# Optimization experiments

Hardware: AMD Instinct MI355X
Metric: run time of the kernel (lower is better)

Reference implementation:

```python
import jax, jax.numpy as jnp
import numpy as np

N, E = 50000, 400000
IN_DIM, TIME_DIM, OUT_DIM, H = 192, 64, 256, 4
D = OUT_DIM // H            # 64 per-head dim
GAT_IN = IN_DIM + TIME_DIM  # 256 == OUT_DIM -> identity residual path


def setup_inputs() -> dict:
    key = jax.random.key(0)
    ks = jax.random.split(key, 9)
    h = jax.random.normal(ks[0], (N, IN_DIM), jnp.float32)
    time_tensor = jax.random.uniform(ks[1], (E,), jnp.float32) * 100.0
    src = jax.random.randint(ks[2], (E,), 0, N, dtype=jnp.int32)
    dst = jax.random.randint(ks[3], (E,), 0, N, dtype=jnp.int32)
    time_w = jax.random.normal(ks[4], (TIME_DIM,), jnp.float32)
    time_b = jax.random.normal(ks[5], (TIME_DIM,), jnp.float32)
    fc_w = jax.random.normal(ks[6], (GAT_IN, H * D), jnp.float32) / np.float32(np.sqrt(GAT_IN))
    attn_l = jax.random.normal(ks[7], (H, D), jnp.float32) * 0.1
    attn_r = jax.random.normal(ks[8], (H, D), jnp.float32) * 0.1
    return {"h": h, "time_tensor": time_tensor, "src": src, "dst": dst,
            "time_w": time_w, "time_b": time_b, "fc_w": fc_w,
            "attn_l": attn_l, "attn_r": attn_r}


def reference(h, time_tensor, src, dst, time_w, time_b, fc_w, attn_l, attn_r):
    # --- temporal encoding per edge: cos(t * w + b) ---
    time_emb = jnp.cos(time_tensor[:, None] * time_w[None, :] + time_b[None, :])  # [E, T]
    # --- mean-aggregate incoming edge time features to nodes (fn.copy_e + fn.mean) ---
    deg = jax.ops.segment_sum(jnp.ones((E,), h.dtype), dst, num_segments=N)       # [N]
    agg_time = jax.ops.segment_sum(time_emb, dst, num_segments=N)
    agg_time = agg_time / jnp.maximum(deg, 1.0)[:, None]                          # [N, T]
    # --- concat node features with aggregated time features ---
    combined = jnp.concatenate([h, agg_time], axis=1)                             # [N, GAT_IN]
    # --- GAT projection and per-node attention logits ---
    feat = (combined @ fc_w).reshape(N, H, D)                                     # [N, H, D]
    el = jnp.einsum('nhd,hd->nh', feat, attn_l)                                   # [N, H]
    er = jnp.einsum('nhd,hd->nh', feat, attn_r)                                   # [N, H]
    # --- edge attention: u_add_v + leaky_relu ---
    e = jax.nn.leaky_relu(el[src] + er[dst], negative_slope=0.01)                 # [E, H]
    # --- edge_softmax over destination segments (numerically stable) ---
    emax = jax.lax.stop_gradient(jax.ops.segment_max(e, dst, num_segments=N))
    emax = jnp.where(jnp.isfinite(emax), emax, 0.0)
    ex = jnp.exp(e - emax[dst])
    denom = jax.ops.segment_sum(ex, dst, num_segments=N)
    a = ex / jnp.maximum(denom[dst], 1e-16)                                       # [E, H]
    # --- u_mul_e + sum aggregation ---
    msg = feat[src] * a[:, :, None]                                               # [E, H, D]
    rst = jax.ops.segment_sum(msg, dst, num_segments=N)                           # [N, H, D]
    # --- identity residual (in_feats == out_feats*num_heads) + elu ---
    rst = rst + combined.reshape(N, H, D)
    rst = jax.nn.elu(rst)
    return rst.reshape(N, OUT_DIM)
```

## Files before the change

kernel.cpp:

```cpp
#include <hip/hip_runtime.h>
#include <hip/hip_bf16.h>
#include <math.h>

#define N_NODES 50000
#define NP      50176
#define N_EDGES 400000
#define IN_DIM  192
#define NB      196

typedef float        f32x4 __attribute__((ext_vector_type(4)));
typedef unsigned int u32x4 __attribute__((ext_vector_type(4)));

__device__ __forceinline__ unsigned short f2bf(float f) {
    union { float f; unsigned int u; } v; v.f = f;
    unsigned int r = (v.u + 0x7FFF + ((v.u >> 16) & 1)) >> 16;
    return (unsigned short)r;
}
__device__ __forceinline__ float bfu_lo(unsigned int u) {
    union { unsigned int u; float f; } v; v.u = u << 16;
    return v.f;
}
__device__ __forceinline__ float bfu_hi(unsigned int u) {
    union { unsigned int u; float f; } v; v.u = u & 0xFFFF0000u;
    return v.f;
}

#define MFMA_BF16(acc, a, b) \
    asm("v_mfma_f32_16x16x32_bf16 %0, %1, %2, %0" : "+v"(acc) : "v"(a), "v"(b))

__global__ void k_hist(const int* __restrict__ dst, int* __restrict__ deg) {
    int e = blockIdx.x * 256 + threadIdx.x;
    if (e >= N_EDGES) return;
    atomicAdd(&deg[dst[e]], 1);
}

__global__ __launch_bounds__(256) void k_scanA(const int* __restrict__ deg,
                                               int* __restrict__ total,
                                               int* __restrict__ start,
                                               int* __restrict__ cursor) {
    __shared__ int part[256];
    __shared__ int base_s;
    int t = threadIdx.x;
    int i = blockIdx.x * 256 + t;
    int v = (i < N_NODES) ? deg[i] : 0;
    part[t] = v;
    __syncthreads();
#pragma unroll
    for (int off = 1; off < 256; off <<= 1) {
        int u = (t >= off) ? part[t - off] : 0;
        __syncthreads();
        part[t] += u;
        __syncthreads();
    }
    if (t == 255) base_s = atomicAdd(total, part[255]);
    __syncthreads();
    if (i < N_NODES) {
        int ex = base_s + part[t] - v;
        start[i] = ex;
        cursor[i] = ex;
    }
}

__global__ void k_bucket(const int* __restrict__ src, const int* __restrict__ dst,
                         const float* __restrict__ time_t, int* __restrict__ cursor,
                         int2* __restrict__ csr2) {
    int e = blockIdx.x * 256 + threadIdx.x;
    if (e >= N_EDGES) return;
    int d = dst[e];
    int idx = atomicAdd(&cursor[d], 1);
    csr2[idx] = make_int2(src[e], __float_as_int(time_t[e]));
}

__global__ void k_prep_w(const float* __restrict__ fw, unsigned short* __restrict__ wF) {
    int tid = blockIdx.x * 256 + threadIdx.x;
    int lane = tid & 63;
    int ks = (tid >> 6) & 7;
    int nt = tid >> 9;
    int c = lane & 15, g = lane >> 4;
    int n = nt * 16 + c;
    int k0 = ks * 32 + g * 8;
    union { unsigned short s[8]; u32x4 v; } u;
#pragma unroll
    for (int j = 0; j < 8; ++j) u.s[j] = f2bf(fw[(size_t)(k0 + j) * 256 + n]);
    *(u32x4*)(wF + (size_t)tid * 8) = u.v;
}

__global__ __launch_bounds__(256) void k_prep_a(const unsigned short* __restrict__ comb,
                                                unsigned short* __restrict__ aF) {
    int tid = blockIdx.x * 256 + threadIdx.x;
    int lane = tid & 63;
    int ks = (tid >> 6) & 7;
    int t = tid >> 9;
    int c = lane & 15, g = lane >> 4;
    u32x4 v = *(const u32x4*)(comb + (size_t)(t * 16 + c) * 256 + ks * 32 + g * 8);
    *(u32x4*)(aF + (size_t)tid * 8) = v;
}

__global__ void k_node_time(const float* __restrict__ h, const int2* __restrict__ csr2,
                            const int* __restrict__ start, const int* __restrict__ deg,
                            const float* __restrict__ tw, const float* __restrict__ tb,
                            unsigned short* __restrict__ comb) {
    int lane = threadIdx.x & 63;
    int wv   = threadIdx.x >> 6;
    int d = blockIdx.x * 4 + wv;
    if (d >= N_NODES) return;
    int k0 = start[d], dg = deg[d];
    float w = tw[lane], b = tb[lane];
    float s = 0.f;
    for (int kc = 0; kc < dg; kc += 64) {
        int cd = min(64, dg - kc);
        float tv = 0.f;
        if (lane < cd) tv = __int_as_float(csr2[k0 + kc + lane].y);
        for (int j = 0; j < cd; ++j) {
            float tj = __shfl(tv, j, 64);
            s += __cosf(tj * w + b);
        }
    }
    float mean = s / fmaxf((float)dg, 1.0f);
    const float* hr = h + (size_t)d * IN_DIM;
    unsigned short* orow = comb + (size_t)d * 256;
    orow[lane]       = f2bf(hr[lane]);
    orow[lane + 64]  = f2bf(hr[lane + 64]);
    orow[lane + 128] = f2bf(hr[lane + 128]);
    orow[lane + 192] = f2bf(mean);
}

__device__ __forceinline__ void gemm_epi(const f32x4 acc[16], int row_lo, int c,
                                         const float* __restrict__ al,
                                         const float* __restrict__ ar,
                                         unsigned short* __restrict__ feat,
                                         float* __restrict__ el,
                                         float* __restrict__ er) {
#pragma unroll
    for (int nt = 0; nt < 16; ++nt) {
#pragma unroll
        for (int reg = 0; reg < 4; ++reg) {
            feat[(size_t)(row_lo + reg) * 256 + nt * 16 + c] = f2bf(acc[nt][reg]);
        }
    }
#pragma unroll
    for (int hh = 0; hh < 4; ++hh) {
        float xl[4] = {0.f, 0.f, 0.f, 0.f};
        float xr[4] = {0.f, 0.f, 0.f, 0.f};
#pragma unroll
        for (int ntl = 0; ntl < 4; ++ntl) {
            int nt = hh * 4 + ntl;
            float av = al[nt * 16 + c];
            float rv = ar[nt * 16 + c];
#pragma unroll
            for (int reg = 0; reg < 4; ++reg) {
                xl[reg] += acc[nt][reg] * av;
                xr[reg] += acc[nt][reg] * rv;
            }
        }
#pragma unroll
        for (int reg = 0; reg < 4; ++reg) {
#pragma unroll
            for (int off = 1; off < 16; off <<= 1) {
                xl[reg] += __shfl_xor(xl[reg], off, 64);
                xr[reg] += __shfl_xor(xr[reg], off, 64);
            }
        }
        if (c == 0) {
#pragma unroll
            for (int reg = 0; reg < 4; ++reg) {
                el[(row_lo + reg) * 4 + hh] = xl[reg];
                er[(row_lo + reg) * 4 + hh] = xr[reg];
            }
        }
    }
}

__global__ __launch_bounds__(512) void k_gemm_mfma(
        const unsigned short* __restrict__ aF,
        const unsigned short* __restrict__ wF,
        const float* __restrict__ al, const float* __restrict__ ar,
        unsigned short* __restrict__ feat,
        float* __restrict__ el, float* __restrict__ er) {
    int lane = threadIdx.x & 63;
    int wave = threadIdx.x >> 6;
    int t0 = blockIdx.x * 16 + wave;
    int c = lane & 15;
    int g = lane >> 4;

    f32x4 acc0[16], acc1[16];
#pragma unroll
    for (int nt = 0; nt < 16; ++nt) {
        acc0[nt] = (f32x4){0.f, 0.f, 0.f, 0.f};
        acc1[nt] = (f32x4){0.f, 0.f, 0.f, 0.f};
    }

    const unsigned short* a0p = aF + ((size_t)(t0 * 8) * 64 + lane) * 8;
    const unsigned short* a1p = aF + ((size_t)((t0 + 8) * 8) * 64 + lane) * 8;
    const unsigned short* bp  = wF + (size_t)lane * 8;

    for (int ks = 0; ks < 8; ++ks) {
        u32x4 a0 = *(const u32x4*)(a0p + ks * 512);
        u32x4 a1 = *(const u32x4*)(a1p + ks * 512);
#pragma unroll
        for (int nt = 0; nt < 16; ++nt) {
            u32x4 b = *(const u32x4*)(bp + (size_t)(nt * 8 + ks) * 512);
            MFMA_BF16(acc0[nt], a0, b);
            MFMA_BF16(acc1[nt], a1, b);
        }
    }

    int row_lo = t0 * 16 + g * 4;
    gemm_epi(acc0, row_lo,       c, al, ar, feat, el, er);
    gemm_epi(acc1, row_lo + 128, c, al, ar, feat, el, er);
}

#define CHUNK 64
__global__ __launch_bounds__(256) void k_node_agg(
        const int2* __restrict__ csr2,
        const int* __restrict__ start, const int* __restrict__ deg,
        const unsigned short* __restrict__ feat, const unsigned short* __restrict__ comb,
        const float* __restrict__ el, const float* __restrict__ er,
        float* __restrict__ out) {
    __shared__ float ex_lds[4][CHUNK * 4];
    __shared__ int   src_lds[4][CHUNK];
    int lane = threadIdx.x & 63;
    int wv   = threadIdx.x >> 6;
    int d = blockIdx.x * 4 + wv;
    int k0 = start[d], k1 = k0 + deg[d];
    int j4 = lane >> 2, h4 = lane & 3;
    int hh = lane >> 4;
    float er_a = er[d * 4 + h4];
    float acc0 = 0.f, acc1 = 0.f, acc2 = 0.f, acc3 = 0.f, den_part = 0.f;

    for (int kc = k0; kc < k1; kc += CHUNK) {
        int cd = min(CHUNK, k1 - kc);
        for (int p = 0; p * 16 < cd; ++p) {
            int j = p * 16 + j4;
            if (j < cd) {
                int s = csr2[kc + j].x;
                if (h4 == 0) src_lds[wv][j] = s;
                float v = el[s * 4 + h4] + er_a;
                v = v > 0.f ? v : 0.01f * v;
                float exv = __expf(v);
                ex_lds[wv][j * 4 + h4] = exv;
                den_part += exv;
            }
        }
#pragma unroll 2
        for (int j = 0; j < cd; ++j) {
            int s = src_lds[wv][j];
            float a = ex_lds[wv][j * 4 + hh];
            const uint2* fp = (const uint2*)(feat + (size_t)s * 256 + lane * 4);
            uint2 u = *fp;
            acc0 += bfu_lo(u.x) * a;
            acc1 += bfu_hi(u.x) * a;
            acc2 += bfu_lo(u.y) * a;
            acc3 += bfu_hi(u.y) * a;
        }
    }
    float dred = den_part;
    dred += __shfl_xor(dred, 4, 64);
    dred += __shfl_xor(dred, 8, 64);
    dred += __shfl_xor(dred, 16, 64);
    dred += __shfl_xor(dred, 32, 64);
    float den = __shfl(dred, hh, 64);
    float inv = 1.0f / fmaxf(den, 1e-16f);

    uint2 cb = *(const uint2*)(comb + (size_t)d * 256 + lane * 4);
    float x0 = bfu_lo(cb.x) + acc0 * inv;
    float x1 = bfu_hi(cb.x) + acc1 * inv;
    float x2 = bfu_lo(cb.y) + acc2 * inv;
    float x3 = bfu_hi(cb.y) + acc3 * inv;
    float4 o;
    o.x = x0 > 0.f ? x0 : expm1f(x0);
    o.y = x1 > 0.f ? x1 : expm1f(x1);
    o.z = x2 > 0.f ? x2 : expm1f(x2);
    o.w = x3 > 0.f ? x3 : expm1f(x3);
    *(float4*)&out[(size_t)d * 256 + lane * 4] = o;
}

extern "C" void kernel_launch(void* const* d_in, const int* in_sizes, int n_in,
                              void* d_out, int out_size, void* d_ws, size_t ws_size,
                              hipStream_t stream) {
    const float* h      = (const float*)d_in[0];
    const float* time_t = (const float*)d_in[1];
    const int*   src    = (const int*)d_in[2];
    const int*   dst    = (const int*)d_in[3];
    const float* tw     = (const float*)d_in[4];
    const float* tb     = (const float*)d_in[5];
    const float* fw     = (const float*)d_in[6];
    const float* al     = (const float*)d_in[7];
    const float* ar     = (const float*)d_in[8];
    float* out = (float*)d_out;

    char* p = (char*)d_ws;
    int*   deg      = (int*)p;                 p += 200000;
    int*   total    = (int*)p;                 p += 64;
    int*   start    = (int*)p;                 p += 200000;
    int*   cursor   = (int*)p;
    unsigned short* wF = (unsigned short*)p;   p += 200000;
    int2*  csr2     = (int2*)p;                p += 3200000;
    unsigned short* comb_bf = (unsigned short*)p; p += (size_t)NP * 512;
    unsigned short* feat_bf = (unsigned short*)p; p += (size_t)NP * 512;
    unsigned short* aF      = (unsigned short*)p; p += (size_t)NP * 512;
    float* el       = (float*)p;               p += (size_t)NP * 16;
    float* er       = (float*)p;               p += (size_t)NP * 16;

    hipMemsetAsync(d_ws, 0, 200064, stream);

    k_hist<<<(N_EDGES + 255) / 256, 256, 0, stream>>>(dst, deg);
    k_scanA<<<NB, 256, 0, stream>>>(deg, total, start, cursor);
    k_bucket<<<(N_EDGES + 255) / 256, 256, 0, stream>>>(src, dst, time_t, cursor, csr2);
    k_prep_w<<<32, 256, 0, stream>>>(fw, wF);
    k_node_time<<<N_NODES / 4, 256, 0, stream>>>(h, csr2, start, deg, tw, tb, comb_bf);
    k_prep_a<<<(NP / 16) * 2, 256, 0, stream>>>(comb_bf, aF);
    k_gemm_mfma<<<NP / 256, 512, 0, stream>>>(aF, wF, al, ar, feat_bf, el, er);
    k_node_agg<<<N_NODES / 4, 256, 0, stream>>>(csr2, start, deg, feat_bf, comb_bf, el, er, out);
}
```

Measured before the change: 157.7 us.

## Fuse weight prep and A-fragment packing into node time kernel

Merges the bf16 weight-fragment conversion and the A-operand fragment packing into the node time-aggregation kernel. Each block now handles 16 nodes, staging their bf16 rows in shared memory and writing the MFMA-ready A layout directly. This removes two kernel launches and the extra global read of the combined buffer by the separate packing pass. In exchange each wave handles four nodes serially, so there are fewer blocks, and the padded rows of the A buffer beyond the node count are no longer written.

```diff
diff --git a/kernel.cpp b/kernel.cpp
--- a/kernel.cpp
+++ b/kernel.cpp
@@ -71,58 +71,67 @@
     csr2[idx] = make_int2(src[e], __float_as_int(time_t[e]));
 }
 
-__global__ void k_prep_w(const float* __restrict__ fw, unsigned short* __restrict__ wF) {
-    int tid = blockIdx.x * 256 + threadIdx.x;
-    int lane = tid & 63;
-    int ks = (tid >> 6) & 7;
-    int nt = tid >> 9;
-    int c = lane & 15, g = lane >> 4;
-    int n = nt * 16 + c;
-    int k0 = ks * 32 + g * 8;
-    union { unsigned short s[8]; u32x4 v; } u;
-#pragma unroll
-    for (int j = 0; j < 8; ++j) u.s[j] = f2bf(fw[(size_t)(k0 + j) * 256 + n]);
-    *(u32x4*)(wF + (size_t)tid * 8) = u.v;
-}
-
-__global__ __launch_bounds__(256) void k_prep_a(const unsigned short* __restrict__ comb,
-                                                unsigned short* __restrict__ aF) {
-    int tid = blockIdx.x * 256 + threadIdx.x;
-    int lane = tid & 63;
-    int ks = (tid >> 6) & 7;
-    int t = tid >> 9;
-    int c = lane & 15, g = lane >> 4;
-    u32x4 v = *(const u32x4*)(comb + (size_t)(t * 16 + c) * 256 + ks * 32 + g * 8);
-    *(u32x4*)(aF + (size_t)tid * 8) = v;
-}
-
-__global__ void k_node_time(const float* __restrict__ h, const int2* __restrict__ csr2,
-                            const int* __restrict__ start, const int* __restrict__ deg,
-                            const float* __restrict__ tw, const float* __restrict__ tb,
-                            unsigned short* __restrict__ comb) {
-    int lane = threadIdx.x & 63;
-    int wv   = threadIdx.x >> 6;
-    int d = blockIdx.x * 4 + wv;
-    if (d >= N_NODES) return;
-    int k0 = start[d], dg = deg[d];
+__global__ __launch_bounds__(256) void k_node_time(
+        const float* __restrict__ h, const int2* __restrict__ csr2,
+        const int* __restrict__ start, const int* __restrict__ deg,
+        const float* __restrict__ tw, const float* __restrict__ tb,
+        const float* __restrict__ fw, unsigned short* __restrict__ wF,
+        unsigned short* __restrict__ comb, unsigned short* __restrict__ aF) {
+    __shared__ unsigned short stage[16][264];
+    int t = threadIdx.x;
+    int lane = t & 63, wv = t >> 6;
+    int bid = blockIdx.x;
+
+    if (bid < 32) {
+        int tid2 = bid * 256 + t;
+        int l2 = tid2 & 63, ks = (tid2 >> 6) & 7, nt = tid2 >> 9;
+        int c = l2 & 15, g = l2 >> 4;
+        int n = nt * 16 + c, k0 = ks * 32 + g * 8;
+        union { unsigned short s[8]; u32x4 v; } u;
+#pragma unroll
+        for (int j = 0; j < 8; ++j) u.s[j] = f2bf(fw[(size_t)(k0 + j) * 256 + n]);
+        *(u32x4*)(wF + (size_t)tid2 * 8) = u.v;
+    }
+
     float w = tw[lane], b = tb[lane];
-    float s = 0.f;
-    for (int kc = 0; kc < dg; kc += 64) {
-        int cd = min(64, dg - kc);
-        float tv = 0.f;
-        if (lane < cd) tv = __int_as_float(csr2[k0 + kc + lane].y);
-        for (int j = 0; j < cd; ++j) {
-            float tj = __shfl(tv, j, 64);
-            s += __cosf(tj * w + b);
-        }
-    }
-    float mean = s / fmaxf((float)dg, 1.0f);
-    const float* hr = h + (size_t)d * IN_DIM;
-    unsigned short* orow = comb + (size_t)d * 256;
-    orow[lane]       = f2bf(hr[lane]);
-    orow[lane + 64]  = f2bf(hr[lane + 64]);
-    orow[lane + 128] = f2bf(hr[lane + 128]);
-    orow[lane + 192] = f2bf(mean);
+    for (int i = 0; i < 4; ++i) {
+        int d = bid * 16 + wv * 4 + i;
+        int k0 = start[d], dg = deg[d];
+        float s = 0.f;
+        for (int kc = 0; kc < dg; kc += 64) {
+            int cd = min(64, dg - kc);
+            float tv = 0.f;
+            if (lane < cd) tv = __int_as_float(csr2[k0 + kc + lane].y);
+            for (int j = 0; j < cd; ++j) {
+                float tj = __shfl(tv, j, 64);
+                s += __cosf(tj * w + b);
+            }
+        }
+        float mean = s / fmaxf((float)dg, 1.0f);
+        const float* hr = h + (size_t)d * IN_DIM;
+        unsigned short v0 = f2bf(hr[lane]);
+        unsigned short v1 = f2bf(hr[lane + 64]);
+        unsigned short v2 = f2bf(hr[lane + 128]);
+        unsigned short v3 = f2bf(mean);
+        unsigned short* orow = comb + (size_t)d * 256;
+        orow[lane]       = v0;
+        orow[lane + 64]  = v1;
+        orow[lane + 128] = v2;
+        orow[lane + 192] = v3;
+        int r = wv * 4 + i;
+        stage[r][lane]       = v0;
+        stage[r][lane + 64]  = v1;
+        stage[r][lane + 128] = v2;
+        stage[r][lane + 192] = v3;
+    }
+    __syncthreads();
+    size_t base = (size_t)bid * 4096;
+#pragma unroll
+    for (int f = t; f < 512; f += 256) {
+        int c = f & 15, g = (f >> 4) & 3, ks = f >> 6;
+        u32x4 v = *(const u32x4*)(&stage[c][ks * 32 + g * 8]);
+        *(u32x4*)(aF + base + (size_t)f * 8) = v;
+    }
 }
 
 __device__ __forceinline__ void gemm_epi(const f32x4 acc[16], int row_lo, int c,
@@ -307,9 +316,7 @@
     k_hist<<<(N_EDGES + 255) / 256, 256, 0, stream>>>(dst, deg);
     k_scanA<<<NB, 256, 0, stream>>>(deg, total, start, cursor);
     k_bucket<<<(N_EDGES + 255) / 256, 256, 0, stream>>>(src, dst, time_t, cursor, csr2);
-    k_prep_w<<<32, 256, 0, stream>>>(fw, wF);
-    k_node_time<<<N_NODES / 4, 256, 0, stream>>>(h, csr2, start, deg, tw, tb, comb_bf);
-    k_prep_a<<<(NP / 16) * 2, 256, 0, stream>>>(comb_bf, aF);
+    k_node_time<<<N_NODES / 16, 256, 0, stream>>>(h, csr2, start, deg, tw, tb, fw, wF, comb_bf, aF);
     k_gemm_mfma<<<NP / 256, 512, 0, stream>>>(aF, wF, al, ar, feat_bf, el, er);
     k_node_agg<<<N_NODES / 4, 256, 0, stream>>>(csr2, start, deg, feat_bf, comb_bf, el, er, out);
 }
```

Result: faster. 148.4 us (-5.8%).
